# Optimization experiments

Measured on AMD Instinct MI355X. Metric: run time of the kernel, lower is better.

## Reference

```python
import jax, jax.numpy as jnp
import numpy as np

B, N, C, K, KS, OC = 8, 4096, 64, 20, 16, 64


def setup_inputs() -> dict:
    key = jax.random.key(0)
    ks = jax.random.split(key, 6)
    return {
        'x': jax.random.normal(ks[0], (B, 3, N), jnp.float32),
        'feature': jax.random.normal(ks[1], (B, C, N), jnp.float32),
        'kernals': jax.random.normal(ks[2], (3, KS), jnp.float32),
        'mlp_w': jax.random.normal(ks[3], (C, 7), jnp.float32) * 0.1,
        'mlp_b': jnp.zeros((C,), jnp.float32),
        'conv_w': jax.random.normal(ks[4], (OC, 2 * C * KS), jnp.float32) * 0.02,
        'conv_b': jnp.zeros((OC,), jnp.float32),
        'bn_gamma': jnp.ones((OC,), jnp.float32),
        'bn_beta': jnp.zeros((OC,), jnp.float32),
    }


def reference(x, feature, kernals, mlp_w, mlp_b, conv_w, conv_b, bn_gamma, bn_beta):
    b, _, n = x.shape
    c = feature.shape[1]
    ksz = kernals.shape[1]
    k = K
    # ---- knn on coords ----
    xt = jnp.swapaxes(x, 1, 2)                      # [B,N,3]
    inner = -2.0 * jnp.einsum('bnc,bmc->bnm', xt, xt)
    xx = jnp.sum(xt * xt, axis=-1)                  # [B,N]
    pd = -xx[:, :, None] - inner - xx[:, None, :]   # negative squared dist
    idx = jax.lax.top_k(pd, k)[1]                   # [B,N,K] nearest (incl. self)
    gather = jax.vmap(lambda pts, i: pts[i])        # per-batch gather
    # ---- geometric features ----
    x_sp = gather(xt, idx)                          # [B,N,K,3]
    x_rel = x_sp - x_sp[:, :, 0:1, :]               # [B,N,K,3]
    x_dis = jnp.linalg.norm(x_rel, axis=-1, keepdims=True)
    center = jnp.broadcast_to(x_sp[:, :, 0:1, :], x_sp.shape)
    x_feats7 = jnp.concatenate([center, x_rel, x_dis], axis=-1)  # [B,N,K,7]
    # Conv1d(7,C,1) == pointwise linear over the 7 channels
    x_feats = jnp.einsum('bnkc,oc->bnok', x_feats7, mlp_w) + mlp_b[None, None, :, None]  # [B,N,C,K]
    # ---- neighbor feature gather ----
    ft = jnp.swapaxes(feature, 1, 2)                # [B,N,C]
    sp_f = gather(ft, idx)                          # [B,N,K,C]
    spirals = jnp.concatenate([jnp.swapaxes(sp_f, 2, 3), x_feats], axis=2)  # [B,N,2C,K]
    # ---- adjacency weights ----
    one_pad = jnp.zeros((k, ksz), jnp.float32).at[0, 0].set(1.0)
    aw = jnp.einsum('bnkc,cs->bnks', x_rel, kernals) + one_pad   # [B,N,K,KS]
    aw = jnp.where(aw > 0, aw, 0.0)
    aw = aw / (jnp.sum(aw, axis=2, keepdims=True) + 1e-6)
    aw = aw * aw
    aw = aw / (jnp.sum(aw, axis=2, keepdims=True) + 1e-6)
    aw = jnp.where(aw > 0.1, aw, 0.0)
    # ---- weighted aggregation + linear ----
    agg = jnp.einsum('bnck,bnks->bncs', spirals, aw)             # [B,N,2C,KS]
    agg = agg.reshape(b, n, 2 * c * ksz)
    out = agg @ conv_w.T + conv_b                                # [B,N,OC]
    out = jnp.swapaxes(out, 1, 2)                                # [B,OC,N]
    # ---- BatchNorm1d (training-mode batch statistics, eps=1e-5) ----
    mean = jnp.mean(out, axis=(0, 2), keepdims=True)
    var = jnp.var(out, axis=(0, 2), keepdims=True)
    out = (out - mean) / jnp.sqrt(var + 1e-5)
    out = out * bn_gamma[None, :, None] + bn_beta[None, :, None]
    return out
```

## Files before the change

kernel.cpp:

```cpp
#include <hip/hip_runtime.h>
#include <cfloat>
#include <math.h>

#define NB 8
#define NPT 4096
#define NC 64
#define KNN 20
#define KSZ 16
#define BPTS 8

typedef __attribute__((ext_vector_type(8))) short short8;
typedef __attribute__((ext_vector_type(4))) float f32x4;

__device__ __forceinline__ unsigned short f2bf(float f) {
  unsigned u = __float_as_uint(f);
  unsigned r = (u + 0x7fffu + ((u >> 16) & 1u)) >> 16;
  return (unsigned short)r;
}
__device__ __forceinline__ float bf2f(unsigned short h) {
  return __uint_as_float(((unsigned)h) << 16);
}

__global__ void k_pack_cw(const float* __restrict__ cw, unsigned short* __restrict__ bp) {
  int t = blockIdx.x * 256 + threadIdx.x;
  int j = t & 7, lane = (t >> 3) & 63, nt = (t >> 9) & 3, ks = t >> 11;
  int k = ks * 32 + ((lane >> 4) << 3) + j;
  int o = nt * 16 + (lane & 15);
  bp[t] = f2bf(cw[o * 2048 + k]);
}

__global__ void k_pack_cw2(const float* __restrict__ cw, const float* __restrict__ mlp_w,
                           const float* __restrict__ mlp_b, unsigned short* __restrict__ bp2) {
  int t = blockIdx.x * 256 + threadIdx.x;
  int jj = t & 7, lane = (t >> 3) & 63, nt = (t >> 9) & 3, ks2 = t >> 11;
  int k = ks2 * 32 + ((lane >> 4) << 3) + jj;
  int s = k >> 3, j = k & 7;
  int o = nt * 16 + (lane & 15);
  float acc = 0.0f;
  for (int c = 0; c < 64; ++c) {
    float coef = (j < 7) ? mlp_w[c * 7 + j] : mlp_b[c];
    acc = fmaf(cw[o * 2048 + 1024 + c * 16 + s], coef, acc);
  }
  bp2[t] = f2bf(acc);
}

__global__ void k_transpose_ft(const float* __restrict__ f, unsigned short* __restrict__ ft) {
  __shared__ float tile[64][65];
  int b = blockIdx.x >> 6;
  int n0 = (blockIdx.x & 63) * 64;
  int lane = threadIdx.x & 63;
  int rr = threadIdx.x >> 6;
#pragma unroll
  for (int c0 = 0; c0 < 64; c0 += 4) {
    int c = c0 + rr;
    tile[c][lane] = f[(b * 64 + c) * 4096 + n0 + lane];
  }
  __syncthreads();
#pragma unroll
  for (int m0 = 0; m0 < 64; m0 += 4) {
    int nn = m0 + rr;
    ft[(b * 4096 + n0 + nn) * 64 + lane] = f2bf(tile[lane][nn]);
  }
}

__device__ __noinline__ void knn_full(const float4* __restrict__ pts, int n, int lane,
                                      int g, int* __restrict__ idxOut) {
  const int M = 24;
  float4 qp = pts[n];
  float qx = qp.x, qy = qp.y, qz = qp.z;
  float v[M];
  int id[M];
#pragma unroll
  for (int r = 0; r < M; ++r) { v[r] = FLT_MAX; id[r] = 0x7fffffff; }
  for (int i = 0; i < 64; ++i) {
    int j = (i << 6) | lane;
    float4 p = pts[j];
    float dx = p.x - qx, dy = p.y - qy, dz = p.z - qz;
    float d2 = fmaf(dx, dx, fmaf(dy, dy, dz * dz));
    bool c[M];
#pragma unroll
    for (int r = 0; r < M; ++r) c[r] = d2 < v[r];
#pragma unroll
    for (int r = M - 1; r >= 1; --r) {
      v[r] = c[r - 1] ? v[r - 1] : (c[r] ? d2 : v[r]);
      id[r] = c[r - 1] ? id[r - 1] : (c[r] ? j : id[r]);
    }
    v[0] = c[0] ? d2 : v[0];
    id[0] = c[0] ? j : id[0];
  }
  unsigned long long key = ((unsigned long long)__float_as_uint(v[0]) << 32) | (unsigned)id[0];
  unsigned long long ext = ~0ull;
  for (int r = 0; r < 24; ++r) {
    unsigned long long k = key;
#pragma unroll
    for (int s = 1; s < 64; s <<= 1) {
      unsigned long long o = __shfl_xor(k, s, 64);
      k = (o < k) ? o : k;
    }
    if (lane == r) ext = k;
    if (key == k) {
#pragma unroll
      for (int q = 0; q < M - 1; ++q) { v[q] = v[q + 1]; id[q] = id[q + 1]; }
      v[M - 1] = FLT_MAX;
      id[M - 1] = 0x7fffffff;
      key = ((unsigned long long)__float_as_uint(v[0]) << 32) | (unsigned)id[0];
    }
  }
  int ei = (int)(unsigned)(ext & 0xffffffffu);
  bool al = lane < 24;
  double dv = -1.0;
  if (al) {
    float4 p = pts[ei];
    double dx = (double)p.x - (double)qx;
    double dy = (double)p.y - (double)qy;
    double dz = (double)p.z - (double)qz;
    dv = dx * dx + dy * dy + dz * dz;
  }
#pragma unroll
  for (int r = 0; r < 4; ++r) {
    double bd = al ? dv : -1.0;
    int bi = al ? ei : -1;
#pragma unroll
    for (int s = 1; s < 64; s <<= 1) {
      double od = __shfl_xor(bd, s, 64);
      int oi = __shfl_xor(bi, s, 64);
      if (od > bd || (od == bd && oi > bi)) { bd = od; bi = oi; }
    }
    if (al && ei == bi) al = false;
  }
  unsigned long long msk = __ballot(al && ei != n);
  if (al) {
    if (ei == n) {
      idxOut[g * 20] = n;
    } else {
      int pos = 1 + __popcll(msk & ((1ull << lane) - 1ull));
      idxOut[g * 20 + pos] = ei;
    }
  }
}

__launch_bounds__(1024, 2)
__global__ void k_knn(const float* __restrict__ x, int* __restrict__ idxOut) {
  __shared__ float4 pts[4096];
  int b = blockIdx.x >> 6;
  const float* xb = x + b * 3 * 4096;
  for (int i = threadIdx.x; i < 4096; i += 1024) {
    float px = xb[i], py = xb[4096 + i], pz = xb[8192 + i];
    pts[i] = make_float4(px, py, pz, fmaf(px, px, fmaf(py, py, pz * pz)));
  }
  __syncthreads();

  int lane = threadIdx.x & 63;
  int w = threadIdx.x >> 6;
  int nb = ((blockIdx.x & 63) << 6) + (w << 2);
  int gb = b * 4096 + nb;

  float m2x[4], m2y[4], m2z[4];
#pragma unroll
  for (int r = 0; r < 4; ++r) {
    float4 q = pts[nb + r];
    m2x[r] = -2.0f * q.x;
    m2y[r] = -2.0f * q.y;
    m2z[r] = -2.0f * q.z;
  }

  float v[4];
#pragma unroll
  for (int r = 0; r < 4; ++r) v[r] = FLT_MAX;
#pragma unroll 2
  for (int i = 0; i < 64; ++i) {
    float4 p = pts[(i << 6) | lane];
#pragma unroll
    for (int r = 0; r < 4; ++r) {
      float d = fmaf(m2z[r], p.z, fmaf(m2y[r], p.y, fmaf(m2x[r], p.x, p.w)));
      v[r] = fminf(v[r], d);
    }
  }

#pragma unroll
  for (int k = 2; k <= 64; k <<= 1) {
#pragma unroll
    for (int j = k >> 1; j > 0; j >>= 1) {
      bool sel = ((lane & k) == 0) == ((lane & j) == 0);
#pragma unroll
      for (int r = 0; r < 4; ++r) {
        float o = __shfl_xor(v[r], j, 64);
        float mn = fminf(v[r], o), mx = fmaxf(v[r], o);
        v[r] = sel ? mn : mx;
      }
    }
  }
  float T[4];
#pragma unroll
  for (int r = 0; r < 4; ++r) T[r] = __shfl(v[r], 23, 64);

  int ei[4], base[4];
  bool ovf[4];
#pragma unroll
  for (int r = 0; r < 4; ++r) { ei[r] = -1; base[r] = 0; ovf[r] = false; }
#pragma unroll 2
  for (int i = 0; i < 64; ++i) {
    float4 p = pts[(i << 6) | lane];
#pragma unroll
    for (int r = 0; r < 4; ++r) {
      float d = fmaf(m2z[r], p.z, fmaf(m2y[r], p.y, fmaf(m2x[r], p.x, p.w)));
      bool pred = (d <= T[r]);
      unsigned long long mask = __ballot(pred);
      if (mask) {
        int cnt = __popcll(mask);
        if (base[r] + cnt > 63) {
          ovf[r] = true;
        } else {
          int dst = pred ? (base[r] + __popcll(mask & ((1ull << lane) - 1ull))) : 63;
          int got = __builtin_amdgcn_ds_permute(dst << 2, (i << 6) | lane);
          bool recv = (lane >= base[r]) && (lane < base[r] + cnt);
          ei[r] = recv ? got : ei[r];
        }
        base[r] += cnt;
      }
    }
  }

#pragma unroll
  for (int r = 0; r < 4; ++r) {
    int n = nb + r, g = gb + r;
    bool ok = !ovf[r];
    if (ok) {
      float4 qp = pts[n];
      bool act = lane < base[r];
      int e = ei[r];
      double dm = 1e300;
      if (act) {
        float4 p = pts[e];
        double dx = (double)p.x - (double)qp.x;
        double dy = (double)p.y - (double)qp.y;
        double dz = (double)p.z - (double)qp.z;
        dm = dx * dx + dy * dy + dz * dz;
      }
      int rank = 0;
      for (int r2 = 0; r2 < base[r]; ++r2) {
        double dr = __shfl(dm, r2, 64);
        int ir = __shfl(e, r2, 64);
        bool less = (dr < dm) || (dr == dm && ir < e);
        rank += less ? 1 : 0;
      }
      bool keep = act && (rank < 20);
      bool isSelf = keep && (e == n);
      unsigned long long smask = __ballot(isSelf);
      ok = (smask != 0ull);
      if (ok) {
        if (isSelf) idxOut[g * 20] = n;
        unsigned long long msk = __ballot(keep && !isSelf);
        if (keep && !isSelf) {
          int pos = 1 + __popcll(msk & ((1ull << lane) - 1ull));
          idxOut[g * 20 + pos] = e;
        }
      }
    }
    if (!ok) knn_full(pts, n, lane, g, idxOut);
  }
}

__launch_bounds__(256, 4)
__global__ void k_main(const float* __restrict__ x, const float* __restrict__ feat,
                       const unsigned short* __restrict__ ftT, int useFtT,
                       const float* __restrict__ kern,
                       const unsigned short* __restrict__ bpk,
                       const unsigned short* __restrict__ bpk2,
                       const float* __restrict__ conv_b, const int* __restrict__ idxIn,
                       float* __restrict__ out) {
  __shared__ __align__(16) unsigned short agg[BPTS][1024];
  __shared__ float awL[BPTS][20][16];
  __shared__ __align__(16) float4 f7s[BPTS][20];
  __shared__ __align__(16) unsigned short fpA[16][128];
  __shared__ __align__(16) float4 qL[BPTS];
  __shared__ int idxL[BPTS][20];

  int t = threadIdx.x;
  int lane = t & 63;
  int w = t >> 6;
  int b = blockIdx.x & 7;
  int n0 = (blockIdx.x >> 3) * BPTS;
  int g0 = b * 4096 + n0;
  const float* xb = x + b * 3 * 4096;

  {
    int pt = t >> 5, slot = t & 31;
    int n = n0 + pt;
    float qx = xb[n], qy = xb[4096 + n], qz = xb[8192 + n];
    if (slot < 20) {
      int kk = idxIn[(g0 + pt) * 20 + slot];
      idxL[pt][slot] = kk;
      float rx = xb[kk] - qx, ry = xb[4096 + kk] - qy, rz = xb[8192 + kk] - qz;
      float ds = sqrtf(rx * rx + ry * ry + rz * rz);
      f7s[pt][slot] = make_float4(rx, ry, rz, ds);
    } else if (slot == 20) {
      qL[pt] = make_float4(qx, qy, qz, 0.0f);
    }
  }
  __syncthreads();

  if (t < 128) {
    int pt = t >> 4, s = t & 15;
    float kx = kern[s], ky = kern[16 + s], kz = kern[32 + s];
    float wv[20];
#pragma unroll
    for (int k = 0; k < 20; ++k) {
      float4 f = f7s[pt][k];
      float dot = f.x * kx + f.y * ky + f.z * kz;
      if (s == 0 && k == 0) dot += 1.0f;
      wv[k] = dot > 0.0f ? dot : 0.0f;
    }
    float sum = 0.0f;
#pragma unroll
    for (int k = 0; k < 20; ++k) sum += wv[k];
    float inv1 = 1.0f / (sum + 1e-6f);
    float sum2 = 0.0f;
#pragma unroll
    for (int k = 0; k < 20; ++k) {
      float u = wv[k] * inv1;
      sum2 += u * u;
    }
    float inv2 = 1.0f / (sum2 + 1e-6f);
    float colsum = 0.0f;
    float F0 = 0.0f, F1 = 0.0f, F2 = 0.0f, F3 = 0.0f;
#pragma unroll
    for (int k = 0; k < 20; ++k) {
      float u = wv[k] * inv1;
      u = u * u * inv2;
      u = (u > 0.1f) ? u : 0.0f;
      awL[pt][k][s] = u;
      colsum += u;
      float4 f = f7s[pt][k];
      F0 = fmaf(f.x, u, F0);
      F1 = fmaf(f.y, u, F1);
      F2 = fmaf(f.z, u, F2);
      F3 = fmaf(f.w, u, F3);
    }
    float4 q = qL[pt];
    __align__(16) unsigned short tmp[8];
    tmp[0] = f2bf(q.x * colsum);
    tmp[1] = f2bf(q.y * colsum);
    tmp[2] = f2bf(q.z * colsum);
    tmp[3] = f2bf(F0);
    tmp[4] = f2bf(F1);
    tmp[5] = f2bf(F2);
    tmp[6] = f2bf(F3);
    tmp[7] = f2bf(colsum);
    *(uint4*)((char*)&fpA[0][0] + pt * 256 + ((s ^ (pt & 7)) << 4)) = *(uint4*)tmp;
  }
  __syncthreads();

#pragma unroll
  for (int half = 0; half < 2; ++half) {
    int pt = (w << 1) + half;
    int c = lane;
    float fv[20];
    if (useFtT) {
#pragma unroll
      for (int k = 0; k < 20; ++k) fv[k] = bf2f(ftT[(b * 4096 + idxL[pt][k]) * 64 + c]);
    } else {
      const float* fb = feat + (b * 64 + c) * 4096;
#pragma unroll
      for (int k = 0; k < 20; ++k) fv[k] = fb[idxL[pt][k]];
    }
    float a1[16];
#pragma unroll
    for (int s = 0; s < 16; ++s) a1[s] = 0.0f;
#pragma unroll
    for (int k = 0; k < 20; ++k) {
      float a = fv[k];
#pragma unroll
      for (int s = 0; s < 16; ++s) a1[s] = fmaf(a, awL[pt][k][s], a1[s]);
    }
    __align__(16) unsigned short tmp[16];
#pragma unroll
    for (int s = 0; s < 16; ++s) tmp[s] = f2bf(a1[s]);
    char* rb = (char*)&agg[pt][0];
    int sw = (pt & 7) << 4;
    *(uint4*)(rb + ((c * 32) ^ sw)) = *(uint4*)&tmp[0];
    *(uint4*)(rb + ((c * 32 + 16) ^ sw)) = *(uint4*)&tmp[8];
  }
  __syncthreads();

  f32x4 acc[4];
#pragma unroll
  for (int nt = 0; nt < 4; ++nt) acc[nt] = (f32x4){0.f, 0.f, 0.f, 0.f};
  {
    int r = lane & 15;
    const char* rowbase = (const char*)&agg[0][0] + r * 2048;
#pragma unroll
    for (int ks = 0; ks < 8; ++ks) {
      int ksl = w * 8 + ks;
      int off = (ksl * 64 + ((lane >> 4) << 4)) ^ ((r & 7) << 4);
      short8 af = *(const short8*)(rowbase + off);
#pragma unroll
      for (int nt = 0; nt < 4; ++nt) {
        short8 bf = *(const short8*)(bpk + (((ksl * 4 + nt) * 64 + lane) << 3));
        acc[nt] = __builtin_amdgcn_mfma_f32_16x16x32_bf16(af, bf, acc[nt], 0, 0, 0);
      }
    }
    {
      int chunk = (w << 2) + (lane >> 4);
      short8 af = *(const short8*)((const char*)&fpA[0][0] + r * 256 + ((chunk ^ (r & 7)) << 4));
#pragma unroll
      for (int nt = 0; nt < 4; ++nt) {
        short8 bf = *(const short8*)(bpk2 + ((((w << 2) + nt) * 64 + lane) << 3));
        acc[nt] = __builtin_amdgcn_mfma_f32_16x16x32_bf16(af, bf, acc[nt], 0, 0, 0);
      }
    }
  }
  __syncthreads();

  float* red = (float*)&agg[0][0];
  {
#pragma unroll
    for (int nt = 0; nt < 4; ++nt)
#pragma unroll
      for (int r = 0; r < 4; ++r) {
        int row = ((lane >> 4) << 2) + r;
        if (row < 8) {
          int o = nt * 16 + (lane & 15);
          red[(w * 8 + row) * 64 + (o ^ ((row & 7) << 2))] = acc[nt][r];
        }
      }
  }
  __syncthreads();
#pragma unroll
  for (int rep = 0; rep < 2; ++rep) {
    int u = rep * 256 + t;
    int pt = u & 7, o = u >> 3;
    float s = conv_b[o];
#pragma unroll
    for (int w2 = 0; w2 < 4; ++w2) s += red[(w2 * 8 + pt) * 64 + (o ^ ((pt & 7) << 2))];
    out[(b * 64 + o) * 4096 + n0 + pt] = s;
  }
}

__global__ void k_bnstats(const float* __restrict__ out, const float* __restrict__ gamma,
                          const float* __restrict__ beta, float* __restrict__ stats) {
  __shared__ double rs[256], rq[256];
  int o = blockIdx.x;
  double s = 0.0, q = 0.0;
  for (int b = 0; b < 8; ++b) {
    const float* p = out + (b * 64 + o) * 4096;
    for (int i = threadIdx.x; i < 4096; i += 256) {
      double v = (double)p[i];
      s += v;
      q += v * v;
    }
  }
  rs[threadIdx.x] = s;
  rq[threadIdx.x] = q;
  __syncthreads();
  for (int st = 128; st > 0; st >>= 1) {
    if ((int)threadIdx.x < st) {
      rs[threadIdx.x] += rs[threadIdx.x + st];
      rq[threadIdx.x] += rq[threadIdx.x + st];
    }
    __syncthreads();
  }
  if (threadIdx.x == 0) {
    double mean = rs[0] / 32768.0;
    double var = rq[0] / 32768.0 - mean * mean;
    double inv = 1.0 / sqrt(var + 1e-5);
    double sc = (double)gamma[o] * inv;
    stats[o * 2] = (float)sc;
    stats[o * 2 + 1] = (float)((double)beta[o] - mean * sc);
  }
}

__global__ void k_bnapply(float* __restrict__ out, const float* __restrict__ stats) {
  int i = blockIdx.x * 256 + threadIdx.x;
  int o = (i >> 12) & 63;
  out[i] = fmaf(out[i], stats[o * 2], stats[o * 2 + 1]);
}

extern "C" void kernel_launch(void* const* d_in, const int* in_sizes, int n_in,
                              void* d_out, int out_size, void* d_ws, size_t ws_size,
                              hipStream_t stream) {
  const float* x = (const float*)d_in[0];
  const float* feat = (const float*)d_in[1];
  const float* kern = (const float*)d_in[2];
  const float* mlp_w = (const float*)d_in[3];
  const float* mlp_b = (const float*)d_in[4];
  const float* conv_w = (const float*)d_in[5];
  const float* conv_b = (const float*)d_in[6];
  const float* gamma = (const float*)d_in[7];
  const float* beta = (const float*)d_in[8];
  float* out = (float*)d_out;
  char* ws = (char*)d_ws;

  int* idx = (int*)ws;
  float* stats = (float*)(ws + 2621440);
  unsigned short* bpk = (unsigned short*)(ws + 2625536);
  unsigned short* bpk2 = (unsigned short*)(ws + 2756608);
  unsigned short* ftT = (unsigned short*)(ws + 2772992);
  int useFtT = (ws_size >= (size_t)(2772992 + 4194304)) ? 1 : 0;

  k_pack_cw<<<256, 256, 0, stream>>>(conv_w, bpk);
  k_pack_cw2<<<32, 256, 0, stream>>>(conv_w, mlp_w, mlp_b, bpk2);
  if (useFtT) k_transpose_ft<<<512, 256, 0, stream>>>(feat, ftT);
  k_knn<<<512, 1024, 0, stream>>>(x, idx);
  k_main<<<4096, 256, 0, stream>>>(x, feat, ftT, useFtT, kern, bpk, bpk2,
                                   conv_b, idx, out);
  k_bnstats<<<64, 256, 0, stream>>>(out, gamma, beta, stats);
  k_bnapply<<<8192, 256, 0, stream>>>(out, stats);
}
```

Baseline: 202.1 us.

## Move neighbor aggregation to MFMA, split BN stats, vectorize BN apply

The per-point neighbor aggregation (features times adjacency weights over K) now runs on bf16 MFMA instead of scalar FMAs. The adjacency weights are stored as bf16 in a fragment-friendly layout padded to 32 neighbors, and shared memory moves into one manually laid-out buffer. BatchNorm statistics are split into a 512-block partial-sum pass plus a tiny finalize kernel, so the reduction is no longer limited to 64 blocks, and the apply kernel uses float4. This adds bf16 rounding of the adjacency weights, a scalarized gather to build the A fragments, and one extra kernel launch.

```diff
diff --git a/kernel.cpp b/kernel.cpp
--- a/kernel.cpp
+++ b/kernel.cpp
@@ -261,6 +261,14 @@
   }
 }
 
+#define AGG_OFF 0
+#define AWB_OFF 16384
+#define FPA_OFF 24576
+#define F7S_OFF 28672
+#define QL_OFF  31232
+#define IDX_OFF 31360
+#define SMEM_SZ 33792
+
 __launch_bounds__(256, 4)
 __global__ void k_main(const float* __restrict__ x, const float* __restrict__ feat,
                        const unsigned short* __restrict__ ftT, int useFtT,
@@ -269,12 +277,12 @@
                        const unsigned short* __restrict__ bpk2,
                        const float* __restrict__ conv_b, const int* __restrict__ idxIn,
                        float* __restrict__ out) {
-  __shared__ __align__(16) unsigned short agg[BPTS][1024];
-  __shared__ float awL[BPTS][20][16];
-  __shared__ __align__(16) float4 f7s[BPTS][20];
-  __shared__ __align__(16) unsigned short fpA[16][128];
-  __shared__ __align__(16) float4 qL[BPTS];
-  __shared__ int idxL[BPTS][20];
+  __shared__ __align__(16) unsigned char smem[SMEM_SZ];
+  unsigned short* agg = (unsigned short*)(smem + AGG_OFF);
+  unsigned short* awB = (unsigned short*)(smem + AWB_OFF);
+  float4* f7s = (float4*)(smem + F7S_OFF);
+  float4* qL = (float4*)(smem + QL_OFF);
+  int* idxL = (int*)(smem + IDX_OFF);
 
   int t = threadIdx.x;
   int lane = t & 63;
@@ -290,10 +298,10 @@
     float qx = xb[n], qy = xb[4096 + n], qz = xb[8192 + n];
     if (slot < 20) {
       int kk = idxIn[(g0 + pt) * 20 + slot];
-      idxL[pt][slot] = kk;
+      idxL[pt * 20 + slot] = kk;
       float rx = xb[kk] - qx, ry = xb[4096 + kk] - qy, rz = xb[8192 + kk] - qz;
       float ds = sqrtf(rx * rx + ry * ry + rz * rz);
-      f7s[pt][slot] = make_float4(rx, ry, rz, ds);
+      f7s[pt * 20 + slot] = make_float4(rx, ry, rz, ds);
     } else if (slot == 20) {
       qL[pt] = make_float4(qx, qy, qz, 0.0f);
     }
@@ -306,7 +314,7 @@
     float wv[20];
 #pragma unroll
     for (int k = 0; k < 20; ++k) {
-      float4 f = f7s[pt][k];
+      float4 f = f7s[pt * 20 + k];
       float dot = f.x * kx + f.y * ky + f.z * kz;
       if (s == 0 && k == 0) dot += 1.0f;
       wv[k] = dot > 0.0f ? dot : 0.0f;
@@ -324,19 +332,23 @@
     float inv2 = 1.0f / (sum2 + 1e-6f);
     float colsum = 0.0f;
     float F0 = 0.0f, F1 = 0.0f, F2 = 0.0f, F3 = 0.0f;
+    unsigned short* awp = awB + pt * 512;
 #pragma unroll
     for (int k = 0; k < 20; ++k) {
       float u = wv[k] * inv1;
       u = u * u * inv2;
       u = (u > 0.1f) ? u : 0.0f;
-      awL[pt][k][s] = u;
+      awp[(((k >> 3) * 16 + s) << 3) + (k & 7)] = f2bf(u);
       colsum += u;
-      float4 f = f7s[pt][k];
+      float4 f = f7s[pt * 20 + k];
       F0 = fmaf(f.x, u, F0);
       F1 = fmaf(f.y, u, F1);
       F2 = fmaf(f.z, u, F2);
       F3 = fmaf(f.w, u, F3);
     }
+#pragma unroll
+    for (int k = 20; k < 32; ++k)
+      awp[(((k >> 3) * 16 + s) << 3) + (k & 7)] = 0;
     float4 q = qL[pt];
     __align__(16) unsigned short tmp[8];
     tmp[0] = f2bf(q.x * colsum);
@@ -347,39 +359,50 @@
     tmp[5] = f2bf(F2);
     tmp[6] = f2bf(F3);
     tmp[7] = f2bf(colsum);
-    *(uint4*)((char*)&fpA[0][0] + pt * 256 + ((s ^ (pt & 7)) << 4)) = *(uint4*)tmp;
-  }
-  __syncthreads();
-
-#pragma unroll
-  for (int half = 0; half < 2; ++half) {
-    int pt = (w << 1) + half;
-    int c = lane;
-    float fv[20];
-    if (useFtT) {
-#pragma unroll
-      for (int k = 0; k < 20; ++k) fv[k] = bf2f(ftT[(b * 4096 + idxL[pt][k]) * 64 + c]);
-    } else {
-      const float* fb = feat + (b * 64 + c) * 4096;
-#pragma unroll
-      for (int k = 0; k < 20; ++k) fv[k] = fb[idxL[pt][k]];
-    }
-    float a1[16];
-#pragma unroll
-    for (int s = 0; s < 16; ++s) a1[s] = 0.0f;
-#pragma unroll
-    for (int k = 0; k < 20; ++k) {
-      float a = fv[k];
-#pragma unroll
-      for (int s = 0; s < 16; ++s) a1[s] = fmaf(a, awL[pt][k][s], a1[s]);
-    }
-    __align__(16) unsigned short tmp[16];
-#pragma unroll
-    for (int s = 0; s < 16; ++s) tmp[s] = f2bf(a1[s]);
-    char* rb = (char*)&agg[pt][0];
-    int sw = (pt & 7) << 4;
-    *(uint4*)(rb + ((c * 32) ^ sw)) = *(uint4*)&tmp[0];
-    *(uint4*)(rb + ((c * 32 + 16) ^ sw)) = *(uint4*)&tmp[8];
+    *(uint4*)(smem + FPA_OFF + pt * 256 + ((s ^ (pt & 7)) << 4)) = *(uint4*)tmp;
+  }
+  __syncthreads();
+
+  {
+    int r15 = lane & 15, chunk = lane >> 4;
+#pragma unroll
+    for (int half = 0; half < 2; ++half) {
+      int pt = (w << 1) + half;
+      int nofs[8];
+#pragma unroll
+      for (int j = 0; j < 8; ++j) {
+        int k = (chunk << 3) + j;
+        nofs[j] = (k < 20) ? ((b * 4096 + idxL[pt * 20 + k]) << 6) : -1;
+      }
+      short8 bfrag = *(const short8*)(awB + pt * 512 + (lane << 3));
+      f32x4 accA[4];
+#pragma unroll
+      for (int ct = 0; ct < 4; ++ct) accA[ct] = (f32x4){0.f, 0.f, 0.f, 0.f};
+#pragma unroll
+      for (int ct = 0; ct < 4; ++ct) {
+        int c = (ct << 4) + r15;
+        union { short8 v; unsigned short u[8]; } af;
+#pragma unroll
+        for (int j = 0; j < 8; ++j) {
+          unsigned short val = 0;
+          if (nofs[j] >= 0) {
+            if (useFtT) val = ftT[nofs[j] + c];
+            else val = f2bf(feat[(b * 64 + c) * 4096 + (nofs[j] >> 6) - b * 4096]);
+          }
+          af.u[j] = val;
+        }
+        accA[ct] = __builtin_amdgcn_mfma_f32_16x16x32_bf16(af.v, bfrag, accA[ct], 0, 0, 0);
+      }
+      char* rb = (char*)(smem + AGG_OFF) + pt * 2048;
+      int sw = (pt & 7) << 4;
+#pragma unroll
+      for (int ct = 0; ct < 4; ++ct)
+#pragma unroll
+        for (int q = 0; q < 4; ++q) {
+          int kidx = (((ct << 4) + (chunk << 2) + q) << 4) + r15;
+          *(unsigned short*)(rb + ((kidx << 1) ^ sw)) = f2bf(accA[ct][q]);
+        }
+    }
   }
   __syncthreads();
 
@@ -388,7 +411,7 @@
   for (int nt = 0; nt < 4; ++nt) acc[nt] = (f32x4){0.f, 0.f, 0.f, 0.f};
   {
     int r = lane & 15;
-    const char* rowbase = (const char*)&agg[0][0] + r * 2048;
+    const char* rowbase = (const char*)(smem + AGG_OFF) + r * 2048;
 #pragma unroll
     for (int ks = 0; ks < 8; ++ks) {
       int ksl = w * 8 + ks;
@@ -402,7 +425,7 @@
     }
     {
       int chunk = (w << 2) + (lane >> 4);
-      short8 af = *(const short8*)((const char*)&fpA[0][0] + r * 256 + ((chunk ^ (r & 7)) << 4));
+      short8 af = *(const short8*)(smem + FPA_OFF + r * 256 + ((chunk ^ (r & 7)) << 4));
 #pragma unroll
       for (int nt = 0; nt < 4; ++nt) {
         short8 bf = *(const short8*)(bpk2 + ((((w << 2) + nt) * 64 + lane) << 3));
@@ -412,7 +435,7 @@
   }
   __syncthreads();
 
-  float* red = (float*)&agg[0][0];
+  float* red = (float*)(smem + AGG_OFF);
   {
 #pragma unroll
     for (int nt = 0; nt < 4; ++nt)
@@ -437,18 +460,15 @@
   }
 }
 
-__global__ void k_bnstats(const float* __restrict__ out, const float* __restrict__ gamma,
-                          const float* __restrict__ beta, float* __restrict__ stats) {
+__global__ void k_bnstats1(const float* __restrict__ out, double* __restrict__ partial) {
   __shared__ double rs[256], rq[256];
-  int o = blockIdx.x;
+  int o = blockIdx.x & 63, b = blockIdx.x >> 6;
+  const float* p = out + (b * 64 + o) * 4096;
   double s = 0.0, q = 0.0;
-  for (int b = 0; b < 8; ++b) {
-    const float* p = out + (b * 64 + o) * 4096;
-    for (int i = threadIdx.x; i < 4096; i += 256) {
-      double v = (double)p[i];
-      s += v;
-      q += v * v;
-    }
+  for (int i = threadIdx.x; i < 4096; i += 256) {
+    double v = (double)p[i];
+    s += v;
+    q += v * v;
   }
   rs[threadIdx.x] = s;
   rq[threadIdx.x] = q;
@@ -461,19 +481,38 @@
     __syncthreads();
   }
   if (threadIdx.x == 0) {
-    double mean = rs[0] / 32768.0;
-    double var = rq[0] / 32768.0 - mean * mean;
-    double inv = 1.0 / sqrt(var + 1e-5);
-    double sc = (double)gamma[o] * inv;
-    stats[o * 2] = (float)sc;
-    stats[o * 2 + 1] = (float)((double)beta[o] - mean * sc);
-  }
+    partial[(o * 8 + b) * 2] = rs[0];
+    partial[(o * 8 + b) * 2 + 1] = rq[0];
+  }
+}
+
+__global__ void k_bnstats2(const double* __restrict__ partial, const float* __restrict__ gamma,
+                           const float* __restrict__ beta, float* __restrict__ stats) {
+  int o = threadIdx.x;
+  double s = 0.0, q = 0.0;
+#pragma unroll
+  for (int b = 0; b < 8; ++b) {
+    s += partial[(o * 8 + b) * 2];
+    q += partial[(o * 8 + b) * 2 + 1];
+  }
+  double mean = s / 32768.0;
+  double var = q / 32768.0 - mean * mean;
+  double inv = 1.0 / sqrt(var + 1e-5);
+  double sc = (double)gamma[o] * inv;
+  stats[o * 2] = (float)sc;
+  stats[o * 2 + 1] = (float)((double)beta[o] - mean * sc);
 }
 
 __global__ void k_bnapply(float* __restrict__ out, const float* __restrict__ stats) {
-  int i = blockIdx.x * 256 + threadIdx.x;
-  int o = (i >> 12) & 63;
-  out[i] = fmaf(out[i], stats[o * 2], stats[o * 2 + 1]);
+  int i4 = blockIdx.x * 256 + threadIdx.x;
+  int o = (i4 >> 10) & 63;
+  float sc = stats[o * 2], sh = stats[o * 2 + 1];
+  float4 v = ((const float4*)out)[i4];
+  v.x = fmaf(v.x, sc, sh);
+  v.y = fmaf(v.y, sc, sh);
+  v.z = fmaf(v.z, sc, sh);
+  v.w = fmaf(v.w, sc, sh);
+  ((float4*)out)[i4] = v;
 }
 
 extern "C" void kernel_launch(void* const* d_in, const int* in_sizes, int n_in,
@@ -492,11 +531,12 @@
   char* ws = (char*)d_ws;
 
   int* idx = (int*)ws;
-  float* stats = (float*)(ws + 2621440);
-  unsigned short* bpk = (unsigned short*)(ws + 2625536);
-  unsigned short* bpk2 = (unsigned short*)(ws + 2756608);
-  unsigned short* ftT = (unsigned short*)(ws + 2772992);
-  int useFtT = (ws_size >= (size_t)(2772992 + 4194304)) ? 1 : 0;
+  double* partial = (double*)(ws + 2621440);
+  float* stats = (float*)(ws + 2629632);
+  unsigned short* bpk = (unsigned short*)(ws + 2633728);
+  unsigned short* bpk2 = (unsigned short*)(ws + 2764800);
+  unsigned short* ftT = (unsigned short*)(ws + 2781184);
+  int useFtT = (ws_size >= (size_t)(2781184 + 4194304)) ? 1 : 0;
 
   k_pack_cw<<<256, 256, 0, stream>>>(conv_w, bpk);
   k_pack_cw2<<<32, 256, 0, stream>>>(conv_w, mlp_w, mlp_b, bpk2);
@@ -504,6 +544,7 @@
   k_knn<<<512, 1024, 0, stream>>>(x, idx);
   k_main<<<4096, 256, 0, stream>>>(x, feat, ftT, useFtT, kern, bpk, bpk2,
                                    conv_b, idx, out);
-  k_bnstats<<<64, 256, 0, stream>>>(out, gamma, beta, stats);
-  k_bnapply<<<8192, 256, 0, stream>>>(out, stats);
-}
+  k_bnstats1<<<512, 256, 0, stream>>>(out, partial);
+  k_bnstats2<<<1, 64, 0, stream>>>(partial, gamma, beta, stats);
+  k_bnapply<<<2048, 256, 0, stream>>>(out, stats);
+}
```

Result: faster. 178.0 us (-11.9%).
